# Optimization experiments

Hardware: AMD Instinct MI355X
Metric: run time of the kernel (lower is better)

Reference implementation:

```python
import jax, jax.numpy as jnp
import numpy as np

B, L, S, H, E, D = 4, 2048, 2048, 8, 64, 64

def setup_inputs() -> dict:
    key = jax.random.key(0)
    kq, kk, kv = jax.random.split(key, 3)
    queries = jax.random.normal(kq, (B, L, H, E), dtype=jnp.float32)
    keys = jax.random.normal(kk, (B, S, H, E), dtype=jnp.float32)
    values = jax.random.normal(kv, (B, S, H, D), dtype=jnp.float32)
    # TriangularCausalMask: True above the diagonal (positions to mask)
    causal = jnp.triu(jnp.ones((L, S), dtype=bool), k=1)
    attn_mask = jnp.broadcast_to(causal[None, None], (B, 1, L, S))
    return {"queries": queries, "keys": keys, "values": values, "attn_mask": attn_mask}

def reference(queries, keys, values, attn_mask):
    scale = 1.0 / jnp.sqrt(jnp.asarray(E, queries.dtype))
    # scores: [B,H,L,S]
    scores = jnp.einsum('blhe,bshe->bhls', queries, keys)
    neg_inf = jnp.asarray(-jnp.inf, scores.dtype)
    scores = jnp.where(attn_mask, neg_inf, scores)
    A = jax.nn.softmax(scale * scores, axis=-1)
    # dropout is identity in eval mode
    V = jnp.einsum('bhls,bshd->blhd', A, values)
    return V
```

## Files before the change

kernel.cpp:

```cpp
#include <hip/hip_runtime.h>
#include <math.h>

typedef __attribute__((ext_vector_type(8))) short bf16x8;
typedef __attribute__((ext_vector_type(4))) float f32x4;
typedef __attribute__((ext_vector_type(4))) unsigned int u32x4;

#define B_ 4
#define L_ 2048
#define S_ 2048
#define H_ 8
#define E_ 64
#define D_ 64
#define NT_ 32
#define TILE_BYTES 16384
#define WS_NEEDED ((size_t)B_ * H_ * NT_ * TILE_BYTES)
#define SCL (0.125f * 1.44269504088896f)

__device__ __forceinline__ unsigned short f2bf(float x) {
    unsigned int u = __builtin_bit_cast(unsigned int, x);
    u += 0x7fffu + ((u >> 16) & 1u);
    return (unsigned short)(u >> 16);
}
__device__ __forceinline__ int rho(int r) {
    return (r & 32) | (((r >> 2) & 1) << 4) | (((r >> 3) & 3) << 2) | (r & 3);
}
__device__ __forceinline__ void gload16(const void* g, void* l) {
    __builtin_amdgcn_global_load_lds((const __attribute__((address_space(1))) unsigned int*)g,
                                     (__attribute__((address_space(3))) unsigned int*)l, 16, 0, 0);
}

__global__ __launch_bounds__(256) void prep_kv(const float* __restrict__ K,
                                               const float* __restrict__ V,
                                               unsigned short* __restrict__ ws)
{
    __shared__ __align__(16) unsigned short vt[64][80];
    const int tid = threadIdx.x;
    const int bid = blockIdx.x;
    const int kt = bid & (NT_ - 1);
    const int bh = bid >> 5;
    const int b  = bh >> 3, h = bh & 7;
    const int s0 = kt * 64;
    const int r  = tid >> 2;
    const int e0 = (tid & 3) * 16;

    const float* krow = K + (((size_t)(b * S_ + s0 + r)) * H_ + h) * E_ + e0;
    const float* vrow = V + (((size_t)(b * S_ + s0 + r)) * H_ + h) * D_ + e0;
    char* tile = (char*)(ws) + ((size_t)bid * TILE_BYTES);

    unsigned short kb[16];
    #pragma unroll
    for (int i = 0; i < 4; ++i) {
        f32x4 k4 = *(const f32x4*)(krow + i * 4);
        #pragma unroll
        for (int j = 0; j < 4; ++j) kb[i * 4 + j] = f2bf(k4[j]);
    }
    {
        const int rr = rho(r);
        const int m  = (rr & 7) << 4;
        char* kbase = tile + rr * 128;
        u32x4 lo, hi;
        #pragma unroll
        for (int j = 0; j < 4; ++j) {
            lo[j] = (unsigned)kb[2 * j] | ((unsigned)kb[2 * j + 1] << 16);
            hi[j] = (unsigned)kb[8 + 2 * j] | ((unsigned)kb[9 + 2 * j] << 16);
        }
        *(u32x4*)(kbase + ((2 * e0) ^ m))      = lo;
        *(u32x4*)(kbase + ((2 * e0 + 16) ^ m)) = hi;
    }
    #pragma unroll
    for (int i = 0; i < 4; ++i) {
        f32x4 v4 = *(const f32x4*)(vrow + i * 4);
        #pragma unroll
        for (int j = 0; j < 4; ++j) vt[e0 + i * 4 + j][r] = f2bf(v4[j]);
    }
    __syncthreads();
    {
        const int d  = tid >> 2;
        const int c0 = (tid & 3) * 16;
        const int m  = (d & 7) << 4;
        char* vbase = tile + 8192 + d * 128;
        u32x4 lo = *(const u32x4*)&vt[d][c0];
        u32x4 hi = *(const u32x4*)&vt[d][c0 + 8];
        *(u32x4*)(vbase + ((2 * c0) ^ m))      = lo;
        *(u32x4*)(vbase + ((2 * c0 + 16) ^ m)) = hi;
    }
}

__global__ __launch_bounds__(128, 3) void attn4(const float* __restrict__ Q,
                                                const unsigned short* __restrict__ ws,
                                                float* __restrict__ O)
{
    __shared__ __align__(16) char lds[2][TILE_BYTES];
    const int tid  = threadIdx.x;
    const int lane = tid & 63;
    const int gr   = tid >> 6;
    const int lq   = lane & 15;
    const int g    = lane >> 4;

    const int bi = blockIdx.x;
    const int p  = bi >> 5;
    const int bh = bi & 31;
    const int b0 = bh >> 3, h = bh & 7;

    const int qt     = gr ? (63 - p) : p;
    const int ntiles = ((63 - p) >> 1) + 1;
    const int dkt    = qt >> 1;
    int qrow[2];
    qrow[0] = qt * 32 + lq;
    qrow[1] = qt * 32 + 16 + lq;

    bf16x8 qf[2][2];
    #pragma unroll
    for (int qs = 0; qs < 2; ++qs) {
        const float* qptr = Q + (((size_t)(b0 * L_ + qrow[qs])) * H_ + h) * E_;
        #pragma unroll
        for (int eb = 0; eb < 2; ++eb) {
            const float* pq = qptr + eb * 32 + g * 8;
            f32x4 a = *(const f32x4*)pq;
            f32x4 b = *(const f32x4*)(pq + 4);
            bf16x8 qv;
            #pragma unroll
            for (int k = 0; k < 4; ++k) {
                qv[k]     = (short)f2bf(a[k] * SCL);
                qv[4 + k] = (short)f2bf(b[k] * SCL);
            }
            qf[qs][eb] = qv;
        }
    }

    f32x4 acc[2][4] = {};
    float ls[2] = {0.f, 0.f};

    const char* tbase = (const char*)ws + (size_t)bh * NT_ * TILE_BYTES;
    #pragma unroll
    for (int i8 = 0; i8 < 8; ++i8)
        gload16(tbase + i8 * 2048 + tid * 16, &lds[0][i8 * 2048 + tid * 16]);

    int cur = 0;
    for (int kt = 0; kt < ntiles; ++kt) {
        if (kt + 1 < ntiles) {
            const char* gp = tbase + (size_t)(kt + 1) * TILE_BYTES;
            char* lp = &lds[cur ^ 1][0];
            #pragma unroll
            for (int i8 = 0; i8 < 8; ++i8)
                gload16(gp + i8 * 2048 + tid * 16, lp + i8 * 2048 + tid * 16);
            asm volatile("s_waitcnt vmcnt(8)" ::: "memory");
        } else {
            asm volatile("s_waitcnt vmcnt(0)" ::: "memory");
        }
        __builtin_amdgcn_s_barrier();
        __builtin_amdgcn_sched_barrier(0);

        const bool active = (gr == 1) || (kt <= dkt);
        if (active) {
            const char* Kl = &lds[cur][0];
            const char* Vl = &lds[cur][8192];
            const int kv0 = kt * 64;

            u32x4 pw[2][2];
            #pragma unroll
            for (int st = 0; st < 4; ++st) {
                const int row = st * 16 + lq;
                const int mm = (row & 7) << 4;
                const char* kr = Kl + row * 128;
                bf16x8 ka0 = *(const bf16x8*)(kr + ((16 * g) ^ mm));
                bf16x8 ka1 = *(const bf16x8*)(kr + ((64 + 16 * g) ^ mm));
                #pragma unroll
                for (int qs = 0; qs < 2; ++qs) {
                    f32x4 z = {0.f, 0.f, 0.f, 0.f};
                    __builtin_amdgcn_s_setprio(1);
                    f32x4 c = __builtin_amdgcn_mfma_f32_16x16x32_bf16(ka0, qf[qs][0], z, 0, 0, 0);
                    c = __builtin_amdgcn_mfma_f32_16x16x32_bf16(ka1, qf[qs][1], c, 0, 0, 0);
                    __builtin_amdgcn_s_setprio(0);
                    if (kt == dkt) {
                        #pragma unroll
                        for (int r = 0; r < 4; ++r) {
                            const int kv = kv0 + 32 * (st >> 1) + 8 * g + 4 * (st & 1) + r;
                            if (kv > qrow[qs]) c[r] = -INFINITY;
                        }
                    }
                    f32x4 ev;
                    #pragma unroll
                    for (int r = 0; r < 4; ++r)
                        asm("v_exp_f32 %0, %1" : "=v"(ev[r]) : "v"(c[r]));
                    ls[qs] += (ev[0] + ev[1]) + (ev[2] + ev[3]);
                    asm("v_cvt_pk_bf16_f32 %0, %1, %2" : "=v"(pw[qs][st >> 1][2 * (st & 1)])     : "v"(ev[0]), "v"(ev[1]));
                    asm("v_cvt_pk_bf16_f32 %0, %1, %2" : "=v"(pw[qs][st >> 1][2 * (st & 1) + 1]) : "v"(ev[2]), "v"(ev[3]));
                }
            }

            #pragma unroll
            for (int dt = 0; dt < 4; ++dt) {
                const int row = dt * 16 + lq;
                const int mm = (row & 7) << 4;
                bf16x8 va0 = *(const bf16x8*)(Vl + row * 128 + ((16 * g) ^ mm));
                bf16x8 va1 = *(const bf16x8*)(Vl + row * 128 + ((64 + 16 * g) ^ mm));
                __builtin_amdgcn_s_setprio(1);
                #pragma unroll
                for (int qs = 0; qs < 2; ++qs) {
                    acc[qs][dt] = __builtin_amdgcn_mfma_f32_16x16x32_bf16(va0, __builtin_bit_cast(bf16x8, pw[qs][0]), acc[qs][dt], 0, 0, 0);
                    acc[qs][dt] = __builtin_amdgcn_mfma_f32_16x16x32_bf16(va1, __builtin_bit_cast(bf16x8, pw[qs][1]), acc[qs][dt], 0, 0, 0);
                }
                __builtin_amdgcn_s_setprio(0);
            }
        }
        __builtin_amdgcn_s_barrier();
        cur ^= 1;
    }

    #pragma unroll
    for (int qs = 0; qs < 2; ++qs) {
        float l = ls[qs] + __shfl_xor(ls[qs], 16);
        l += __shfl_xor(l, 32);
        const float inv = 1.0f / l;
        float* op = O + (((size_t)(b0 * L_ + qrow[qs])) * H_ + h) * D_;
        #pragma unroll
        for (int dt = 0; dt < 4; ++dt) {
            f32x4 o;
            #pragma unroll
            for (int r = 0; r < 4; ++r) o[r] = acc[qs][dt][r] * inv;
            *(f32x4*)(op + dt * 16 + 4 * g) = o;
        }
    }
}

#define KPITCH 72
__global__ __launch_bounds__(256, 2) void attn_fwd_fb(
    const float* __restrict__ Q, const float* __restrict__ K,
    const float* __restrict__ V, float* __restrict__ O)
{
    __shared__ unsigned short Klds[64 * KPITCH];
    __shared__ unsigned short Vlds[64 * KPITCH];
    const int tid = threadIdx.x, lane = tid & 63, w = tid >> 6;
    const int lq = lane & 15, g = lane >> 4;
    const int bid = blockIdx.x, qb = bid & 31, bh = bid >> 5;
    const int b0 = bh >> 3, h = bh & 7;
    const int q0 = qb * 64, qrow = q0 + w * 16 + lq;
    const float* qptr = Q + ((size_t)(b0 * L_ + qrow) * H_ + h) * E_;
    bf16x8 qf[2];
    #pragma unroll
    for (int eb = 0; eb < 2; ++eb) {
        const float* p = qptr + eb * 32 + g * 8;
        f32x4 a = *(const f32x4*)p; f32x4 b = *(const f32x4*)(p + 4);
        bf16x8 q;
        #pragma unroll
        for (int j = 0; j < 4; ++j) { q[j] = (short)f2bf(a[j] * 0.125f); q[4 + j] = (short)f2bf(b[j] * 0.125f); }
        qf[eb] = q;
    }
    const int tr = tid >> 2, tc = tid & 3;
    const int rh = rho(tr);
    f32x4 acc[4] = {};
    float mrow = -INFINITY, lrow = 0.f;
    for (int kt = 0; kt < qb + 1; ++kt) {
        const int kv0 = kt * 64;
        __syncthreads();
        {
            const float* krow = K + ((size_t)((b0 * S_ + kv0 + tr)) * H_ + h) * E_;
            const float* vrow = V + ((size_t)((b0 * S_ + kv0 + tr)) * H_ + h) * D_;
            #pragma unroll
            for (int i = 0; i < 4; ++i) {
                const int e0 = tc * 4 + i * 16;
                f32x4 k4 = *(const f32x4*)(krow + e0);
                unsigned int lo = (unsigned)f2bf(k4[0]) | ((unsigned)f2bf(k4[1]) << 16);
                unsigned int hi = (unsigned)f2bf(k4[2]) | ((unsigned)f2bf(k4[3]) << 16);
                *(uint2*)&Klds[rh * KPITCH + e0] = make_uint2(lo, hi);
                f32x4 v4 = *(const f32x4*)(vrow + e0);
                #pragma unroll
                for (int k2 = 0; k2 < 4; ++k2) Vlds[(e0 + k2) * KPITCH + tr] = f2bf(v4[k2]);
            }
        }
        __syncthreads();
        f32x4 sc[4];
        #pragma unroll
        for (int st = 0; st < 4; ++st) {
            const unsigned short* kr = &Klds[(st * 16 + lq) * KPITCH];
            bf16x8 ka0 = *(const bf16x8*)(kr + 8 * g);
            bf16x8 ka1 = *(const bf16x8*)(kr + 32 + 8 * g);
            f32x4 c = {0.f, 0.f, 0.f, 0.f};
            c = __builtin_amdgcn_mfma_f32_16x16x32_bf16(ka0, qf[0], c, 0, 0, 0);
            c = __builtin_amdgcn_mfma_f32_16x16x32_bf16(ka1, qf[1], c, 0, 0, 0);
            sc[st] = c;
        }
        float tmax = -INFINITY;
        #pragma unroll
        for (int st = 0; st < 4; ++st) {
            const int kvb = kv0 + 32 * (st >> 1) + 8 * g + 4 * (st & 1);
            #pragma unroll
            for (int r = 0; r < 4; ++r) { if (kvb + r > qrow) sc[st][r] = -INFINITY; tmax = fmaxf(tmax, sc[st][r]); }
        }
        tmax = fmaxf(tmax, __shfl_xor(tmax, 16));
        tmax = fmaxf(tmax, __shfl_xor(tmax, 32));
        const float mnew = fmaxf(mrow, tmax);
        const float corr = __expf(mrow - mnew);
        float p[4][4]; float tsum = 0.f;
        #pragma unroll
        for (int st = 0; st < 4; ++st)
            #pragma unroll
            for (int r = 0; r < 4; ++r) { float e = __expf(sc[st][r] - mnew); p[st][r] = e; tsum += e; }
        tsum += __shfl_xor(tsum, 16); tsum += __shfl_xor(tsum, 32);
        lrow = lrow * corr + tsum; mrow = mnew;
        #pragma unroll
        for (int dt = 0; dt < 4; ++dt)
            #pragma unroll
            for (int r = 0; r < 4; ++r) acc[dt][r] *= corr;
        bf16x8 pb[2];
        #pragma unroll
        for (int bb = 0; bb < 2; ++bb)
            #pragma unroll
            for (int s = 0; s < 2; ++s)
                #pragma unroll
                for (int r = 0; r < 4; ++r) pb[bb][4 * s + r] = (short)f2bf(p[2 * bb + s][r]);
        #pragma unroll
        for (int bb = 0; bb < 2; ++bb)
            #pragma unroll
            for (int dt = 0; dt < 4; ++dt) {
                bf16x8 va = *(const bf16x8*)&Vlds[(dt * 16 + lq) * KPITCH + 32 * bb + 8 * g];
                acc[dt] = __builtin_amdgcn_mfma_f32_16x16x32_bf16(va, pb[bb], acc[dt], 0, 0, 0);
            }
    }
    const float inv = 1.0f / lrow;
    float* optr = O + ((size_t)(b0 * L_ + qrow) * H_ + h) * D_;
    #pragma unroll
    for (int dt = 0; dt < 4; ++dt) {
        f32x4 o;
        #pragma unroll
        for (int r = 0; r < 4; ++r) o[r] = acc[dt][r] * inv;
        *(f32x4*)(optr + dt * 16 + 4 * g) = o;
    }
}

extern "C" void kernel_launch(void* const* d_in, const int* in_sizes, int n_in,
                              void* d_out, int out_size, void* d_ws, size_t ws_size,
                              hipStream_t stream) {
    const float* Q = (const float*)d_in[0];
    const float* K = (const float*)d_in[1];
    const float* V = (const float*)d_in[2];
    float* O = (float*)d_out;
    if (ws_size >= WS_NEEDED) {
        prep_kv<<<dim3(B_ * H_ * NT_), 256, 0, stream>>>(K, V, (unsigned short*)d_ws);
        attn4<<<dim3(B_ * H_ * 32), 128, 0, stream>>>(Q, (const unsigned short*)d_ws, O);
    } else {
        attn_fwd_fb<<<dim3(B_ * H_ * 32), 256, 0, stream>>>(Q, K, V, O);
    }
}
```

Measured before the change: 49.44 us.

## Load K/V tiles straight into registers, dropping LDS staging and barriers

The attention kernel no longer stages K/V tiles through double-buffered LDS with block barriers. Each wave now loads its own MFMA operand fragments from the prepared bf16 workspace directly into registers, issuing the next tile's K and V loads while the current tile computes. Work is regrouped into 256-thread blocks of four independent waves, each handling one 32-row query tile with its own causal tile count (paired for balance), and the grid is 512 blocks. This removes LDS traffic and barrier stalls. In exchange, every wave re-fetches the same tile from global/L2, and register pressure rises.

```diff
diff --git a/kernel.cpp b/kernel.cpp
--- a/kernel.cpp
+++ b/kernel.cpp
@@ -23,10 +23,6 @@
 }
 __device__ __forceinline__ int rho(int r) {
     return (r & 32) | (((r >> 2) & 1) << 4) | (((r >> 3) & 3) << 2) | (r & 3);
-}
-__device__ __forceinline__ void gload16(const void* g, void* l) {
-    __builtin_amdgcn_global_load_lds((const __attribute__((address_space(1))) unsigned int*)g,
-                                     (__attribute__((address_space(3))) unsigned int*)l, 16, 0, 0);
 }
 
 __global__ __launch_bounds__(256) void prep_kv(const float* __restrict__ K,
@@ -86,25 +82,26 @@
     }
 }
 
-__global__ __launch_bounds__(128, 3) void attn4(const float* __restrict__ Q,
+#define GL16(dst, p, o) asm volatile("global_load_dwordx4 %0, %1, off offset:" o \
+                                     : "=v"(dst) : "v"(p) : "memory")
+
+__global__ __launch_bounds__(256, 2) void attn5(const float* __restrict__ Q,
                                                 const unsigned short* __restrict__ ws,
                                                 float* __restrict__ O)
 {
-    __shared__ __align__(16) char lds[2][TILE_BYTES];
     const int tid  = threadIdx.x;
     const int lane = tid & 63;
-    const int gr   = tid >> 6;
+    const int w    = tid >> 6;
     const int lq   = lane & 15;
     const int g    = lane >> 4;
 
-    const int bi = blockIdx.x;
-    const int p  = bi >> 5;
-    const int bh = bi & 31;
-    const int b0 = bh >> 3, h = bh & 7;
-
-    const int qt     = gr ? (63 - p) : p;
-    const int ntiles = ((63 - p) >> 1) + 1;
-    const int dkt    = qt >> 1;
+    const int bid = blockIdx.x;
+    const int bh  = bid & 31;
+    const int j   = bid >> 5;
+    const int b0  = bh >> 3, h = bh & 7;
+
+    const int qt = (w & 2) ? (62 - 2 * j + (w & 1)) : (2 * j + (w & 1));
+    const int nt = (qt >> 1) + 1;
     int qrow[2];
     qrow[0] = qt * 32 + lq;
     qrow[1] = qt * 32 + 16 + lq;
@@ -128,84 +125,105 @@
         }
     }
 
+    const char* tb = (const char*)ws + (size_t)bh * NT_ * TILE_BYTES;
+    const int mm  = (lq & 7) << 4;
+    const int o_a = lq * 128 + ((16 * g) ^ mm) + 3072;
+    const int o_b = lq * 128 + ((64 + 16 * g) ^ mm) + 3072;
+    const char* pKa = tb + o_a;
+    const char* pKb = tb + o_b;
+    const char* pVa = tb + 8192 + o_a;
+    const char* pVb = tb + 8192 + o_b;
+
+    u32x4 ka[8], vb[8];
     f32x4 acc[2][4] = {};
     float ls[2] = {0.f, 0.f};
 
-    const char* tbase = (const char*)ws + (size_t)bh * NT_ * TILE_BYTES;
-    #pragma unroll
-    for (int i8 = 0; i8 < 8; ++i8)
-        gload16(tbase + i8 * 2048 + tid * 16, &lds[0][i8 * 2048 + tid * 16]);
-
-    int cur = 0;
-    for (int kt = 0; kt < ntiles; ++kt) {
-        if (kt + 1 < ntiles) {
-            const char* gp = tbase + (size_t)(kt + 1) * TILE_BYTES;
-            char* lp = &lds[cur ^ 1][0];
-            #pragma unroll
-            for (int i8 = 0; i8 < 8; ++i8)
-                gload16(gp + i8 * 2048 + tid * 16, lp + i8 * 2048 + tid * 16);
-            asm volatile("s_waitcnt vmcnt(8)" ::: "memory");
-        } else {
-            asm volatile("s_waitcnt vmcnt(0)" ::: "memory");
-        }
-        __builtin_amdgcn_s_barrier();
+    GL16(ka[0], pKa, "-3072"); GL16(ka[1], pKb, "-3072");
+    GL16(ka[2], pKa, "-1024"); GL16(ka[3], pKb, "-1024");
+    GL16(ka[4], pKa, "1024");  GL16(ka[5], pKb, "1024");
+    GL16(ka[6], pKa, "3072");  GL16(ka[7], pKb, "3072");
+    GL16(vb[0], pVa, "-3072"); GL16(vb[1], pVb, "-3072");
+    GL16(vb[2], pVa, "-1024"); GL16(vb[3], pVb, "-1024");
+    GL16(vb[4], pVa, "1024");  GL16(vb[5], pVb, "1024");
+    GL16(vb[6], pVa, "3072");  GL16(vb[7], pVb, "3072");
+
+    for (int kt = 0; kt < nt; ++kt) {
+        const bool notlast = (kt + 1 < nt);
+
+        asm volatile("s_waitcnt vmcnt(8)" ::: "memory");
         __builtin_amdgcn_sched_barrier(0);
 
-        const bool active = (gr == 1) || (kt <= dkt);
-        if (active) {
-            const char* Kl = &lds[cur][0];
-            const char* Vl = &lds[cur][8192];
-            const int kv0 = kt * 64;
-
-            u32x4 pw[2][2];
+        f32x4 sc[2][4];
+        __builtin_amdgcn_s_setprio(1);
+        #pragma unroll
+        for (int st = 0; st < 4; ++st) {
+            bf16x8 ka0 = __builtin_bit_cast(bf16x8, ka[2 * st]);
+            bf16x8 ka1 = __builtin_bit_cast(bf16x8, ka[2 * st + 1]);
+            #pragma unroll
+            for (int qs = 0; qs < 2; ++qs) {
+                f32x4 z = {0.f, 0.f, 0.f, 0.f};
+                f32x4 c = __builtin_amdgcn_mfma_f32_16x16x32_bf16(ka0, qf[qs][0], z, 0, 0, 0);
+                sc[qs][st] = __builtin_amdgcn_mfma_f32_16x16x32_bf16(ka1, qf[qs][1], c, 0, 0, 0);
+            }
+        }
+        __builtin_amdgcn_s_setprio(0);
+
+        if (notlast) {
+            pKa += TILE_BYTES; pKb += TILE_BYTES;
+            GL16(ka[0], pKa, "-3072"); GL16(ka[1], pKb, "-3072");
+            GL16(ka[2], pKa, "-1024"); GL16(ka[3], pKb, "-1024");
+            GL16(ka[4], pKa, "1024");  GL16(ka[5], pKb, "1024");
+            GL16(ka[6], pKa, "3072");  GL16(ka[7], pKb, "3072");
+        }
+
+        const int kv0 = kt * 64;
+        u32x4 pw[2][2];
+        #pragma unroll
+        for (int qs = 0; qs < 2; ++qs) {
             #pragma unroll
             for (int st = 0; st < 4; ++st) {
-                const int row = st * 16 + lq;
-                const int mm = (row & 7) << 4;
-                const char* kr = Kl + row * 128;
-                bf16x8 ka0 = *(const bf16x8*)(kr + ((16 * g) ^ mm));
-                bf16x8 ka1 = *(const bf16x8*)(kr + ((64 + 16 * g) ^ mm));
+                f32x4 c = sc[qs][st];
+                if (kt == nt - 1) {
+                    #pragma unroll
+                    for (int r = 0; r < 4; ++r) {
+                        const int kv = kv0 + 32 * (st >> 1) + 8 * g + 4 * (st & 1) + r;
+                        if (kv > qrow[qs]) c[r] = -INFINITY;
+                    }
+                }
+                f32x4 ev;
                 #pragma unroll
-                for (int qs = 0; qs < 2; ++qs) {
-                    f32x4 z = {0.f, 0.f, 0.f, 0.f};
-                    __builtin_amdgcn_s_setprio(1);
-                    f32x4 c = __builtin_amdgcn_mfma_f32_16x16x32_bf16(ka0, qf[qs][0], z, 0, 0, 0);
-                    c = __builtin_amdgcn_mfma_f32_16x16x32_bf16(ka1, qf[qs][1], c, 0, 0, 0);
-                    __builtin_amdgcn_s_setprio(0);
-                    if (kt == dkt) {
-                        #pragma unroll
-                        for (int r = 0; r < 4; ++r) {
-                            const int kv = kv0 + 32 * (st >> 1) + 8 * g + 4 * (st & 1) + r;
-                            if (kv > qrow[qs]) c[r] = -INFINITY;
-                        }
-                    }
-                    f32x4 ev;
-                    #pragma unroll
-                    for (int r = 0; r < 4; ++r)
-                        asm("v_exp_f32 %0, %1" : "=v"(ev[r]) : "v"(c[r]));
-                    ls[qs] += (ev[0] + ev[1]) + (ev[2] + ev[3]);
-                    asm("v_cvt_pk_bf16_f32 %0, %1, %2" : "=v"(pw[qs][st >> 1][2 * (st & 1)])     : "v"(ev[0]), "v"(ev[1]));
-                    asm("v_cvt_pk_bf16_f32 %0, %1, %2" : "=v"(pw[qs][st >> 1][2 * (st & 1) + 1]) : "v"(ev[2]), "v"(ev[3]));
-                }
-            }
-
-            #pragma unroll
-            for (int dt = 0; dt < 4; ++dt) {
-                const int row = dt * 16 + lq;
-                const int mm = (row & 7) << 4;
-                bf16x8 va0 = *(const bf16x8*)(Vl + row * 128 + ((16 * g) ^ mm));
-                bf16x8 va1 = *(const bf16x8*)(Vl + row * 128 + ((64 + 16 * g) ^ mm));
-                __builtin_amdgcn_s_setprio(1);
-                #pragma unroll
-                for (int qs = 0; qs < 2; ++qs) {
-                    acc[qs][dt] = __builtin_amdgcn_mfma_f32_16x16x32_bf16(va0, __builtin_bit_cast(bf16x8, pw[qs][0]), acc[qs][dt], 0, 0, 0);
-                    acc[qs][dt] = __builtin_amdgcn_mfma_f32_16x16x32_bf16(va1, __builtin_bit_cast(bf16x8, pw[qs][1]), acc[qs][dt], 0, 0, 0);
-                }
-                __builtin_amdgcn_s_setprio(0);
-            }
-        }
-        __builtin_amdgcn_s_barrier();
-        cur ^= 1;
+                for (int r = 0; r < 4; ++r)
+                    asm("v_exp_f32 %0, %1" : "=v"(ev[r]) : "v"(c[r]));
+                ls[qs] += (ev[0] + ev[1]) + (ev[2] + ev[3]);
+                asm("v_cvt_pk_bf16_f32 %0, %1, %2" : "=v"(pw[qs][st >> 1][2 * (st & 1)])     : "v"(ev[0]), "v"(ev[1]));
+                asm("v_cvt_pk_bf16_f32 %0, %1, %2" : "=v"(pw[qs][st >> 1][2 * (st & 1) + 1]) : "v"(ev[2]), "v"(ev[3]));
+            }
+        }
+
+        if (notlast) asm volatile("s_waitcnt vmcnt(8)" ::: "memory");
+        else         asm volatile("s_waitcnt vmcnt(0)" ::: "memory");
+        __builtin_amdgcn_sched_barrier(0);
+
+        __builtin_amdgcn_s_setprio(1);
+        #pragma unroll
+        for (int dt = 0; dt < 4; ++dt) {
+            bf16x8 va0 = __builtin_bit_cast(bf16x8, vb[2 * dt]);
+            bf16x8 va1 = __builtin_bit_cast(bf16x8, vb[2 * dt + 1]);
+            #pragma unroll
+            for (int qs = 0; qs < 2; ++qs) {
+                acc[qs][dt] = __builtin_amdgcn_mfma_f32_16x16x32_bf16(va0, __builtin_bit_cast(bf16x8, pw[qs][0]), acc[qs][dt], 0, 0, 0);
+                acc[qs][dt] = __builtin_amdgcn_mfma_f32_16x16x32_bf16(va1, __builtin_bit_cast(bf16x8, pw[qs][1]), acc[qs][dt], 0, 0, 0);
+            }
+        }
+        __builtin_amdgcn_s_setprio(0);
+
+        if (notlast) {
+            pVa += TILE_BYTES; pVb += TILE_BYTES;
+            GL16(vb[0], pVa, "-3072"); GL16(vb[1], pVb, "-3072");
+            GL16(vb[2], pVa, "-1024"); GL16(vb[3], pVb, "-1024");
+            GL16(vb[4], pVa, "1024");  GL16(vb[5], pVb, "1024");
+            GL16(vb[6], pVa, "3072");  GL16(vb[7], pVb, "3072");
+        }
     }
 
     #pragma unroll
@@ -244,7 +262,7 @@
         f32x4 a = *(const f32x4*)p; f32x4 b = *(const f32x4*)(p + 4);
         bf16x8 q;
         #pragma unroll
-        for (int j = 0; j < 4; ++j) { q[j] = (short)f2bf(a[j] * 0.125f); q[4 + j] = (short)f2bf(b[j] * 0.125f); }
+        for (int jq = 0; jq < 4; ++jq) { q[jq] = (short)f2bf(a[jq] * 0.125f); q[4 + jq] = (short)f2bf(b[jq] * 0.125f); }
         qf[eb] = q;
     }
     const int tr = tid >> 2, tc = tid & 3;
@@ -338,7 +356,7 @@
     float* O = (float*)d_out;
     if (ws_size >= WS_NEEDED) {
         prep_kv<<<dim3(B_ * H_ * NT_), 256, 0, stream>>>(K, V, (unsigned short*)d_ws);
-        attn4<<<dim3(B_ * H_ * 32), 128, 0, stream>>>(Q, (const unsigned short*)d_ws, O);
+        attn5<<<dim3(512), 256, 0, stream>>>(Q, (const unsigned short*)d_ws, O);
     } else {
         attn_fwd_fb<<<dim3(B_ * H_ * 32), 256, 0, stream>>>(Q, K, V, O);
     }
```

After: 46.11 us. 6.7% less time.
